# Optimization experiments

Measured on AMD Instinct MI355X. Metric: run time of the kernel, lower is better.

The kernel has to match this reference:

```python
import jax, jax.numpy as jnp
import numpy as np
import math

NUM_SYN = 1000
NUM_MEM = 100
TAU_MIN, TAU_MAX = 10.0, 1000.0
TAU_S = 5.0
DELTA_T = 1.0
LAMBDA = 3.0

def _kappas():
    kappa_s = np.float32(np.exp(-DELTA_T / TAU_S))  # scalar (tau_s uniform)
    tau_m = np.logspace(math.log10(TAU_MIN + 1e-06), math.log10(TAU_MAX - 1e-06), NUM_MEM)
    kappa_m = np.exp(-DELTA_T / np.clip(tau_m, 1e-06, None)).astype(np.float32)
    return kappa_s, jnp.asarray(kappa_m)

def custom_tanh(x):
    return jnp.tanh(x * (2.0 / 3.0)) * 1.7159

def setup_inputs() -> dict:
    key = jax.random.key(0)
    ks = jax.random.split(key, 5)
    B, T = 128, 1024
    H = 2 * NUM_MEM  # 200
    X = jax.random.normal(ks[0], (B, T, NUM_SYN), dtype=jnp.float32)
    w_s = jnp.full((NUM_SYN,), 0.5, dtype=jnp.float32)
    W1 = jax.random.normal(ks[1], (NUM_SYN + NUM_MEM, H), dtype=jnp.float32) * 0.03
    b1 = jnp.zeros((H,), dtype=jnp.float32)
    W2 = jax.random.normal(ks[2], (H, NUM_MEM), dtype=jnp.float32) * 0.07
    b2 = jnp.zeros((NUM_MEM,), dtype=jnp.float32)
    Wy = jax.random.normal(ks[3], (NUM_MEM, 10), dtype=jnp.float32) * 0.1
    by = jnp.zeros((10,), dtype=jnp.float32)
    return {"X": X, "w_s": w_s, "W1": W1, "b1": b1, "W2": W2, "b2": b2, "Wy": Wy, "by": by}

def reference(X, w_s, W1, b1, W2, b2, Wy, by):
    kappa_s, kappa_m = _kappas()
    B = X.shape[0]
    w_s_pos = jax.nn.relu(w_s)

    def step(carry, x_t):
        s, m = carry  # s: [B, S], m: [B, M]
        s = kappa_s * s + w_s_pos * x_t
        km = kappa_m * m
        inp = jnp.concatenate([s, km], axis=-1)  # [B, S+M]
        h = jax.nn.relu(inp @ W1 + b1)
        dm = custom_tanh(h @ W2 + b2)
        m = km + LAMBDA * (1.0 - kappa_m) * dm
        y = m @ Wy + by
        return (s, m), y

    s0 = jnp.zeros((B, NUM_SYN), dtype=X.dtype)
    m0 = jnp.zeros((B, NUM_MEM), dtype=X.dtype)
    Xt = jnp.swapaxes(X, 0, 1)  # [T, B, S]
    _, ys = jax.lax.scan(step, (s0, m0), Xt)
    return jnp.swapaxes(ys, 0, 1)  # [B, T, num_output]
```

## Files before the change

### kernel.cpp

```cpp
#include <hip/hip_runtime.h>
#include <math.h>

#define SDIM 1000
#define KPAD 1024
#define HDIM 200
#define MDIM 100
#define NPAD 208
#define TSTEPS 1024
#define BATCH 128
#define MT (BATCH*TSTEPS)
#define TOTX ((size_t)MT*(size_t)SDIM)

#define Z_OFF 458752

typedef _Float16 half2_t __attribute__((ext_vector_type(2)));
typedef __attribute__((ext_vector_type(8))) short short8;
typedef __attribute__((ext_vector_type(4))) float f32x4;

static __device__ __forceinline__ unsigned short f2bf(float f) {
    unsigned u = __float_as_uint(f);
    unsigned r = 0x7fffu + ((u >> 16) & 1u);
    return (unsigned short)((u + r) >> 16);
}
static __device__ __forceinline__ float bf2f(unsigned short h) {
    return __uint_as_float((unsigned)h << 16);
}
static __device__ __forceinline__ half2_t as_h2(unsigned v) {
    union { unsigned u; half2_t h; } c; c.u = v; return c.h;
}
static __device__ __forceinline__ unsigned as_u32(half2_t h) {
    union { half2_t h; unsigned u; } c; c.h = h; return c.u;
}
static __device__ __forceinline__ half2_t pk2(float a, float b) {
    half2_t r; r[0] = (_Float16)a; r[1] = (_Float16)b; return r;
}

static __device__ __forceinline__ void wg_barrier() {
    asm volatile("s_waitcnt lgkmcnt(0)" ::: "memory");
    __builtin_amdgcn_s_barrier();
    asm volatile("" ::: "memory");
}

__global__ __launch_bounds__(256) void prep_wpt(const float* __restrict__ w_s,
                                                const float* __restrict__ W1,
                                                unsigned short* __restrict__ wpt) {
    int idx = blockIdx.x * 256 + threadIdx.x;
    int n = idx >> 10, k = idx & (KPAD - 1);
    float v = 0.f;
    if (n < HDIM && k < SDIM) {
        float ws = fmaxf(w_s[k], 0.f);
        v = ws * W1[k * HDIM + n];
    }
    wpt[idx] = f2bf(v);
}

__global__ __launch_bounds__(256) void gemm_z(const float* __restrict__ X,
                                              const unsigned short* __restrict__ wpt,
                                              unsigned short* __restrict__ Z) {
    __shared__ __align__(16) unsigned short Abuf[2][128][40];
    __shared__ __align__(16) unsigned short Bbuf[2][13][16][40];
    const int t = threadIdx.x;
    const int m0 = blockIdx.x * 128;
    const int lane = t & 63, w = t >> 6;

    f32x4 acc[2][13];
#pragma unroll
    for (int mt = 0; mt < 2; ++mt)
#pragma unroll
        for (int i = 0; i < 13; ++i) acc[mt][i] = (f32x4){0.f, 0.f, 0.f, 0.f};

    auto stageA = [&](int bsel, int k0) {
        const int row = t >> 1, half = t & 1;
        size_t g = (size_t)(m0 + row) * SDIM + (size_t)(k0 + half * 16);
        float4 f0{}, f1{}, f2{}, f3{};
        if (g + 15 < TOTX) {
            f0 = *(const float4*)(X + g);      f1 = *(const float4*)(X + g + 4);
            f2 = *(const float4*)(X + g + 8);  f3 = *(const float4*)(X + g + 12);
        }
        short8 p0, p1;
        p0[0]=(short)f2bf(f0.x); p0[1]=(short)f2bf(f0.y); p0[2]=(short)f2bf(f0.z); p0[3]=(short)f2bf(f0.w);
        p0[4]=(short)f2bf(f1.x); p0[5]=(short)f2bf(f1.y); p0[6]=(short)f2bf(f1.z); p0[7]=(short)f2bf(f1.w);
        p1[0]=(short)f2bf(f2.x); p1[1]=(short)f2bf(f2.y); p1[2]=(short)f2bf(f2.z); p1[3]=(short)f2bf(f2.w);
        p1[4]=(short)f2bf(f3.x); p1[5]=(short)f2bf(f3.y); p1[6]=(short)f2bf(f3.z); p1[7]=(short)f2bf(f3.w);
        *(short8*)&Abuf[bsel][row][half * 16]     = p0;
        *(short8*)&Abuf[bsel][row][half * 16 + 8] = p1;
    };
    auto stageB = [&](int bsel, int k0) {
#pragma unroll
        for (int j = 0; j < 4; ++j) {
            int e = t + 256 * j;
            if (e < 832) {
                int n = e >> 2, q = e & 3;
                short8 v = *(const short8*)(wpt + (size_t)n * KPAD + k0 + q * 8);
                *(short8*)&Bbuf[bsel][n >> 4][n & 15][q * 8] = v;
            }
        }
    };

    stageA(0, 0);
    stageB(0, 0);
#pragma unroll 1
    for (int it = 0; it < 32; ++it) {
        __syncthreads();
        if (it + 1 < 32) { stageA((it + 1) & 1, (it + 1) * 32); stageB((it + 1) & 1, (it + 1) * 32); }
        const int bsel = it & 1;
        const short8 av0 = *(const short8*)&Abuf[bsel][w * 32 + (lane & 15)][(lane >> 4) * 8];
        const short8 av1 = *(const short8*)&Abuf[bsel][w * 32 + 16 + (lane & 15)][(lane >> 4) * 8];
#pragma unroll
        for (int nt = 0; nt < 13; ++nt) {
            const short8 bv = *(const short8*)&Bbuf[bsel][nt][lane & 15][(lane >> 4) * 8];
            acc[0][nt] = __builtin_amdgcn_mfma_f32_16x16x32_bf16(av0, bv, acc[0][nt], 0, 0, 0);
            acc[1][nt] = __builtin_amdgcn_mfma_f32_16x16x32_bf16(av1, bv, acc[1][nt], 0, 0, 0);
        }
    }

    const int colb = lane & 15;
#pragma unroll
    for (int mt = 0; mt < 2; ++mt) {
        const int rowb = m0 + w * 32 + mt * 16 + (lane >> 4) * 4;
#pragma unroll
        for (int nt = 0; nt < 13; ++nt) {
            int col = nt * 16 + colb;
            if (col < HDIM) {
#pragma unroll
                for (int r = 0; r < 4; ++r)
                    Z[(size_t)(rowb + r) * HDIM + col] = f2bf(acc[mt][nt][r]);
            }
        }
    }
}

__global__ __launch_bounds__(256, 1) void scan_seq(const unsigned short* __restrict__ Z,
        const float* __restrict__ W1, const float* __restrict__ b1,
        const float* __restrict__ W2, const float* __restrict__ b2,
        const float* __restrict__ Wy, const float* __restrict__ by,
        float* __restrict__ out) {
    __shared__ __align__(16) float part[2][4][104];
    __shared__ float kap_s[104], cm_s[104];

    const int t = threadIdx.x;
    const int b = blockIdx.x;
    const int w = t >> 6, lane = t & 63;
    const int n = 50 * w + lane;
    const bool hAct = lane < 50;
    const bool yAct = (w == 0) && (lane >= 50 && lane < 60);
    const int o = lane - 50;

    if (t < 104) {
        float kv = 0.f, cv = 0.f;
        if (t < MDIM) {
            double lg = 1.0000000434294482
                      + (double)t * ((2.9999999995657055 - 1.0000000434294482) / 99.0);
            double tau = exp(lg * 2.302585092994046);
            kv = (float)exp(-1.0 / tau);
            cv = 3.0f * (1.0f - kv);
        }
        kap_s[t] = kv; cm_s[t] = cv;
    }
    __syncthreads();

    half2_t w1r[50];
#pragma unroll
    for (int c = 0; c < 50; ++c) {
        float a0 = 0.f, a1 = 0.f;
        if (hAct) {
            a0 = kap_s[2 * c]     * W1[(SDIM + 2 * c)     * HDIM + n];
            a1 = kap_s[2 * c + 1] * W1[(SDIM + 2 * c + 1) * HDIM + n];
        } else if (yAct) {
            a0 = Wy[(2 * c) * 10 + o];
            a1 = Wy[(2 * c + 1) * 10 + o];
        }
        w1r[c] = pk2(a0, a1);
    }
    float base_b = hAct ? b1[n] : (yAct ? by[o] : 0.f);

    const int j0 = 2 * lane, j1 = 2 * lane + 1;
    half2_t w2r[50];
#pragma unroll
    for (int c = 0; c < 25; ++c) {
        float a00 = 0.f, a10 = 0.f, a01 = 0.f, a11 = 0.f;
        if (hAct) {
            int k0 = 50 * w + 2 * c, k1 = k0 + 1;
            a00 = W2[k0 * MDIM + j0]; a10 = W2[k1 * MDIM + j0];
            a01 = W2[k0 * MDIM + j1]; a11 = W2[k1 * MDIM + j1];
        }
        w2r[2 * c]     = pk2(a00, a10);
        w2r[2 * c + 1] = pk2(a01, a11);
    }

    float kap0 = 0.f, kap1 = 0.f, cm0 = 0.f, cm1 = 0.f, b20 = 0.f, b21 = 0.f;
    if (hAct) {
        kap0 = kap_s[j0]; kap1 = kap_s[j1];
        cm0 = cm_s[j0];   cm1 = cm_s[j1];
        b20 = b2[j0];     b21 = b2[j1];
    }

    const unsigned short* Zb = Z + (size_t)b * TSTEPS * HDIM;
    float* outb = out + (size_t)b * TSTEPS * 10;

    float u = 0.f, m0 = 0.f, m1 = 0.f;
    unsigned short zA = 0, zB = 0;
    if (hAct) { zA = Zb[n]; zB = Zb[HDIM + n]; }

    int sm[50];
#pragma unroll
    for (int c = 0; c < 50; ++c) sm[c] = 0;

    __syncthreads();

    auto stepf = [&](const int P, unsigned short& zreg, const int st) {
        float acc = base_b;
        if (hAct) {
            u = 0.81873075307798182f * u + bf2f(zreg);
            int stn = st + 2; stn = (stn < TSTEPS) ? stn : TSTEPS - 1;
            zreg = Zb[(size_t)stn * HDIM + n];
            acc += u;
        }
        float r = acc;
        if (hAct || yAct) {
#pragma unroll
            for (int c = 0; c < 50; ++c)
                r = __builtin_amdgcn_fdot2(w1r[c], as_h2((unsigned)sm[c]), r, false);
        }
        if (yAct && st > 0) outb[(size_t)(st - 1) * 10 + o] = r;
        float h = fmaxf(r, 0.f);

        float ho = __shfl_xor(h, 1);
        unsigned hpk = as_u32(pk2(h, ho));
        int sh[25];
#pragma unroll
        for (int c = 0; c < 25; ++c) sh[c] = __builtin_amdgcn_readlane((int)hpk, 2 * c);

        if (hAct) {
            float a0 = 0.f, a1 = 0.f;
#pragma unroll
            for (int c = 0; c < 25; ++c) {
                a0 = __builtin_amdgcn_fdot2(w2r[2 * c],     as_h2((unsigned)sh[c]), a0, false);
                a1 = __builtin_amdgcn_fdot2(w2r[2 * c + 1], as_h2((unsigned)sh[c]), a1, false);
            }
            *(float2*)&part[P][w][j0] = make_float2(a0, a1);
        }
        wg_barrier();

        if (hAct) {
            float2 q0 = *(const float2*)&part[P][0][j0];
            float2 q1 = *(const float2*)&part[P][1][j0];
            float2 q2 = *(const float2*)&part[P][2][j0];
            float2 q3 = *(const float2*)&part[P][3][j0];
            float s0 = ((q0.x + q1.x) + (q2.x + q3.x)) + b20;
            float s1 = ((q0.y + q1.y) + (q2.y + q3.y)) + b21;
            float x0 = s0 * (2.f / 3.f), x1 = s1 * (2.f / 3.f);
            float e0 = __expf(2.f * x0), e1 = __expf(2.f * x1);
            float dm0 = 1.7159f * (1.f - 2.f / (e0 + 1.f));
            float dm1 = 1.7159f * (1.f - 2.f / (e1 + 1.f));
            m0 = kap0 * m0 + cm0 * dm0;
            m1 = kap1 * m1 + cm1 * dm1;
        }
        unsigned mpk = as_u32(pk2(m0, m1));
#pragma unroll
        for (int c = 0; c < 50; ++c) sm[c] = __builtin_amdgcn_readlane((int)mpk, c);
    };

#pragma unroll 1
    for (int st = 0; st < TSTEPS; st += 2) {
        stepf(0, zA, st);
        stepf(1, zB, st + 1);
    }

    if (yAct) {
        float r = base_b;
#pragma unroll
        for (int c = 0; c < 50; ++c)
            r = __builtin_amdgcn_fdot2(w1r[c], as_h2((unsigned)sm[c]), r, false);
        outb[(size_t)(TSTEPS - 1) * 10 + o] = r;
    }
}

extern "C" void kernel_launch(void* const* d_in, const int* in_sizes, int n_in,
                              void* d_out, int out_size, void* d_ws, size_t ws_size,
                              hipStream_t stream) {
    const float* X  = (const float*)d_in[0];
    const float* ws = (const float*)d_in[1];
    const float* W1 = (const float*)d_in[2];
    const float* b1 = (const float*)d_in[3];
    const float* W2 = (const float*)d_in[4];
    const float* b2 = (const float*)d_in[5];
    const float* Wy = (const float*)d_in[6];
    const float* by = (const float*)d_in[7];
    float* out = (float*)d_out;

    unsigned short* wpt = (unsigned short*)d_ws;
    unsigned short* Z   = (unsigned short*)((char*)d_ws + Z_OFF);

    hipLaunchKernelGGL(prep_wpt, dim3((NPAD * KPAD) / 256), dim3(256), 0, stream, ws, W1, wpt);
    hipLaunchKernelGGL(gemm_z, dim3(MT / 128), dim3(256), 0, stream, X, wpt, Z);
    hipLaunchKernelGGL(scan_seq, dim3(BATCH), dim3(256), 0, stream,
                       Z, W1, b1, W2, b2, Wy, by, out);
}
```

Baseline: 1.038 ms.

## Batch 16 sequences per block in scan and use MFMA for recurrent matmuls

Replaces the per-sequence scan kernel (one block per batch element using fdot2 and readlane broadcasts) with a kernel that processes 16 batch elements per block. The recurrent W1, W2 and Wy products become 16x16x32 f16 MFMA operations, with h and m exchanged through LDS. This cuts the launch to 8 blocks, trading parallelism across CUs for much denser per-step math. The tanh is also rewritten using exp2 and rcp with a prescaled bias.

```diff
diff --git a/kernel.cpp b/kernel.cpp
--- a/kernel.cpp
+++ b/kernel.cpp
@@ -14,6 +14,7 @@
 #define Z_OFF 458752
 
 typedef _Float16 half2_t __attribute__((ext_vector_type(2)));
+typedef _Float16 f16x8 __attribute__((ext_vector_type(8)));
 typedef __attribute__((ext_vector_type(8))) short short8;
 typedef __attribute__((ext_vector_type(4))) float f32x4;
 
@@ -21,18 +22,6 @@
     unsigned u = __float_as_uint(f);
     unsigned r = 0x7fffu + ((u >> 16) & 1u);
     return (unsigned short)((u + r) >> 16);
-}
-static __device__ __forceinline__ float bf2f(unsigned short h) {
-    return __uint_as_float((unsigned)h << 16);
-}
-static __device__ __forceinline__ half2_t as_h2(unsigned v) {
-    union { unsigned u; half2_t h; } c; c.u = v; return c.h;
-}
-static __device__ __forceinline__ unsigned as_u32(half2_t h) {
-    union { half2_t h; unsigned u; } c; c.h = h; return c.u;
-}
-static __device__ __forceinline__ half2_t pk2(float a, float b) {
-    half2_t r; r[0] = (_Float16)a; r[1] = (_Float16)b; return r;
 }
 
 static __device__ __forceinline__ void wg_barrier() {
@@ -130,149 +119,236 @@
     }
 }
 
-__global__ __launch_bounds__(256, 1) void scan_seq(const unsigned short* __restrict__ Z,
+#define MSTR 136
+#define HSTR 232
+#define KEXP 1.9235933878519513f
+#define KSF  0.81873075307798182f
+
+__global__ __launch_bounds__(256, 1) void scan_mfma(
+        const unsigned short* __restrict__ Z,
         const float* __restrict__ W1, const float* __restrict__ b1,
         const float* __restrict__ W2, const float* __restrict__ b2,
         const float* __restrict__ Wy, const float* __restrict__ by,
         float* __restrict__ out) {
-    __shared__ __align__(16) float part[2][4][104];
-    __shared__ float kap_s[104], cm_s[104];
+    __shared__ __align__(16) _Float16 mbuf[16 * MSTR];
+    __shared__ __align__(16) _Float16 hbuf[16 * HSTR];
+    __shared__ float kap_s[128];
 
     const int t = threadIdx.x;
-    const int b = blockIdx.x;
+    const int bg = blockIdx.x;
     const int w = t >> 6, lane = t & 63;
-    const int n = 50 * w + lane;
-    const bool hAct = lane < 50;
-    const bool yAct = (w == 0) && (lane >= 50 && lane < 60);
-    const int o = lane - 50;
-
-    if (t < 104) {
-        float kv = 0.f, cv = 0.f;
+    const int c = lane & 15, g = lane >> 4;
+
+    if (t < 128) {
+        float kv = 0.f;
         if (t < MDIM) {
             double lg = 1.0000000434294482
                       + (double)t * ((2.9999999995657055 - 1.0000000434294482) / 99.0);
             double tau = exp(lg * 2.302585092994046);
             kv = (float)exp(-1.0 / tau);
-            cv = 3.0f * (1.0f - kv);
-        }
-        kap_s[t] = kv; cm_s[t] = cv;
-    }
+        }
+        kap_s[t] = kv;
+    }
+    for (int idx = t; idx < 16 * MSTR; idx += 256) mbuf[idx] = (_Float16)0.f;
+    for (int idx = t; idx < 16 * HSTR; idx += 256) hbuf[idx] = (_Float16)0.f;
     __syncthreads();
 
-    half2_t w1r[50];
-#pragma unroll
-    for (int c = 0; c < 50; ++c) {
-        float a0 = 0.f, a1 = 0.f;
-        if (hAct) {
-            a0 = kap_s[2 * c]     * W1[(SDIM + 2 * c)     * HDIM + n];
-            a1 = kap_s[2 * c + 1] * W1[(SDIM + 2 * c + 1) * HDIM + n];
-        } else if (yAct) {
-            a0 = Wy[(2 * c) * 10 + o];
-            a1 = Wy[(2 * c + 1) * 10 + o];
-        }
-        w1r[c] = pk2(a0, a1);
-    }
-    float base_b = hAct ? b1[n] : (yAct ? by[o] : 0.f);
-
-    const int j0 = 2 * lane, j1 = 2 * lane + 1;
-    half2_t w2r[50];
-#pragma unroll
-    for (int c = 0; c < 25; ++c) {
-        float a00 = 0.f, a10 = 0.f, a01 = 0.f, a11 = 0.f;
-        if (hAct) {
-            int k0 = 50 * w + 2 * c, k1 = k0 + 1;
-            a00 = W2[k0 * MDIM + j0]; a10 = W2[k1 * MDIM + j0];
-            a01 = W2[k0 * MDIM + j1]; a11 = W2[k1 * MDIM + j1];
-        }
-        w2r[2 * c]     = pk2(a00, a10);
-        w2r[2 * c + 1] = pk2(a01, a11);
-    }
-
-    float kap0 = 0.f, kap1 = 0.f, cm0 = 0.f, cm1 = 0.f, b20 = 0.f, b21 = 0.f;
-    if (hAct) {
-        kap0 = kap_s[j0]; kap1 = kap_s[j1];
-        cm0 = cm_s[j0];   cm1 = cm_s[j1];
-        b20 = b2[j0];     b21 = b2[j1];
-    }
-
-    const unsigned short* Zb = Z + (size_t)b * TSTEPS * HDIM;
-    float* outb = out + (size_t)b * TSTEPS * 10;
-
-    float u = 0.f, m0 = 0.f, m1 = 0.f;
-    unsigned short zA = 0, zB = 0;
-    if (hAct) { zA = Zb[n]; zB = Zb[HDIM + n]; }
-
-    int sm[50];
-#pragma unroll
-    for (int c = 0; c < 50; ++c) sm[c] = 0;
-
+    const int base1 = (w == 0) ? 0 : (1 + 3 * w);
+    const int n1 = (w == 0) ? 4 : 3;
+    const int base2 = 2 * w;
+    const int n2 = (w == 3) ? 1 : 2;
+    const bool isw3 = (w == 3);
+
+    f16x8 w1f[4][4];
+    float b1c[4][4];
+    f32x4 u[4];
+#pragma unroll
+    for (int i = 0; i < 4; ++i) {
+        const int T = base1 + i;
+        const int n = 16 * T + c;
+        const bool tv = (i < n1);
+#pragma unroll
+        for (int ks = 0; ks < 4; ++ks)
+#pragma unroll
+            for (int e = 0; e < 8; ++e) {
+                int k = 32 * ks + 8 * g + e;
+                float v = (tv && k < MDIM && n < HDIM)
+                        ? kap_s[k] * W1[(SDIM + k) * HDIM + n] : 0.f;
+                w1f[i][ks][e] = (_Float16)v;
+            }
+#pragma unroll
+        for (int r = 0; r < 4; ++r) {
+            int nr = 16 * T + 4 * g + r;
+            b1c[i][r] = (tv && nr < HDIM) ? b1[nr] : 0.f;
+        }
+        u[i] = (f32x4){0.f, 0.f, 0.f, 0.f};
+    }
+
+    f16x8 w2f[2][7];
+    float kapc[2][4], cmc[2][4], b2kc[2][4], mst[2][4];
+#pragma unroll
+    for (int j = 0; j < 2; ++j) {
+        const int Tj = base2 + j;
+        const int mj = 16 * Tj + c;
+        const bool jv = (j < n2);
+#pragma unroll
+        for (int ks = 0; ks < 7; ++ks)
+#pragma unroll
+            for (int e = 0; e < 8; ++e) {
+                int k = 32 * ks + 8 * g + e;
+                float v = (jv && k < HDIM && mj < MDIM) ? W2[k * MDIM + mj] : 0.f;
+                w2f[j][ks][e] = (_Float16)v;
+            }
+#pragma unroll
+        for (int r = 0; r < 4; ++r) {
+            int mr = 16 * Tj + 4 * g + r;
+            bool mv = jv && (mr < MDIM);
+            float kv = mv ? kap_s[mr] : 0.f;
+            kapc[j][r] = kv;
+            cmc[j][r]  = mv ? 3.f * (1.f - kv) : 0.f;
+            b2kc[j][r] = mv ? b2[mr] * KEXP : 0.f;
+            mst[j][r]  = 0.f;
+        }
+    }
+
+    f16x8 wyf[4];
+    float byc[4];
+#pragma unroll
+    for (int ks = 0; ks < 4; ++ks)
+#pragma unroll
+        for (int e = 0; e < 8; ++e) {
+            int k = 32 * ks + 8 * g + e;
+            wyf[ks][e] = (_Float16)((isw3 && c < 10 && k < MDIM) ? Wy[k * 10 + c] : 0.f);
+        }
+#pragma unroll
+    for (int r = 0; r < 4; ++r) {
+        int o = 4 * g + r;
+        byc[r] = (isw3 && o < 10) ? by[o] : 0.f;
+    }
+
+    const unsigned short* Zc = Z + (size_t)(bg * 16 + c) * (TSTEPS * HDIM);
+    float* outc = out + (size_t)(bg * 16 + c) * (TSTEPS * 10);
+
+    uint2 zA[4], zB[4];
+#pragma unroll
+    for (int i = 0; i < 4; ++i) {
+        const int n0 = 16 * (base1 + i) + 4 * g;
+        const bool zv = (i < n1) && (n0 < HDIM);
+        zA[i] = zv ? *(const uint2*)(Zc + 0 * HDIM + n0) : make_uint2(0u, 0u);
+        zB[i] = zv ? *(const uint2*)(Zc + 1 * HDIM + n0) : make_uint2(0u, 0u);
+    }
     __syncthreads();
 
-    auto stepf = [&](const int P, unsigned short& zreg, const int st) {
-        float acc = base_b;
-        if (hAct) {
-            u = 0.81873075307798182f * u + bf2f(zreg);
-            int stn = st + 2; stn = (stn < TSTEPS) ? stn : TSTEPS - 1;
-            zreg = Zb[(size_t)stn * HDIM + n];
-            acc += u;
-        }
-        float r = acc;
-        if (hAct || yAct) {
-#pragma unroll
-            for (int c = 0; c < 50; ++c)
-                r = __builtin_amdgcn_fdot2(w1r[c], as_h2((unsigned)sm[c]), r, false);
-        }
-        if (yAct && st > 0) outb[(size_t)(st - 1) * 10 + o] = r;
-        float h = fmaxf(r, 0.f);
-
-        float ho = __shfl_xor(h, 1);
-        unsigned hpk = as_u32(pk2(h, ho));
-        int sh[25];
-#pragma unroll
-        for (int c = 0; c < 25; ++c) sh[c] = __builtin_amdgcn_readlane((int)hpk, 2 * c);
-
-        if (hAct) {
-            float a0 = 0.f, a1 = 0.f;
-#pragma unroll
-            for (int c = 0; c < 25; ++c) {
-                a0 = __builtin_amdgcn_fdot2(w2r[2 * c],     as_h2((unsigned)sh[c]), a0, false);
-                a1 = __builtin_amdgcn_fdot2(w2r[2 * c + 1], as_h2((unsigned)sh[c]), a1, false);
-            }
-            *(float2*)&part[P][w][j0] = make_float2(a0, a1);
+    auto stepf = [&](uint2 (&zr)[4], const int st) {
+        f16x8 bm[4];
+#pragma unroll
+        for (int ks = 0; ks < 4; ++ks)
+            bm[ks] = *(const f16x8*)(&mbuf[c * MSTR + 8 * g + 32 * ks]);
+
+        f32x4 acc1[4];
+#pragma unroll
+        for (int i = 0; i < 4; ++i) {
+            uint2 zv = zr[i];
+            u[i][0] = fmaf(KSF, u[i][0], __uint_as_float(zv.x << 16));
+            u[i][1] = fmaf(KSF, u[i][1], __uint_as_float(zv.x & 0xffff0000u));
+            u[i][2] = fmaf(KSF, u[i][2], __uint_as_float(zv.y << 16));
+            u[i][3] = fmaf(KSF, u[i][3], __uint_as_float(zv.y & 0xffff0000u));
+            acc1[i][0] = u[i][0] + b1c[i][0];
+            acc1[i][1] = u[i][1] + b1c[i][1];
+            acc1[i][2] = u[i][2] + b1c[i][2];
+            acc1[i][3] = u[i][3] + b1c[i][3];
+            const int n0 = 16 * (base1 + i) + 4 * g;
+            if ((i < n1) && (n0 < HDIM)) {
+                int stn = st + 2; stn = (stn < TSTEPS) ? stn : TSTEPS - 1;
+                zr[i] = *(const uint2*)(Zc + (size_t)stn * HDIM + n0);
+            }
+        }
+
+#pragma unroll
+        for (int i = 0; i < 4; ++i) {
+            if (i < n1) {
+#pragma unroll
+                for (int ks = 0; ks < 4; ++ks)
+                    acc1[i] = __builtin_amdgcn_mfma_f32_16x16x32_f16(
+                                  w1f[i][ks], bm[ks], acc1[i], 0, 0, 0);
+            }
+        }
+
+        if (isw3) {
+            f32x4 ya = (f32x4){0.f, 0.f, 0.f, 0.f};
+#pragma unroll
+            for (int ks = 0; ks < 4; ++ks)
+                ya = __builtin_amdgcn_mfma_f32_16x16x32_f16(wyf[ks], bm[ks], ya, 0, 0, 0);
+            if (st > 0) {
+#pragma unroll
+                for (int r = 0; r < 4; ++r) {
+                    int o = 4 * g + r;
+                    if (o < 10)
+                        outc[(size_t)(st - 1) * 10 + o] = ya[r] + byc[r];
+                }
+            }
+        }
+
+#pragma unroll
+        for (int i = 0; i < 4; ++i) {
+            if (i < n1) {
+                unsigned p0 = __builtin_bit_cast(unsigned,
+                    __builtin_amdgcn_cvt_pkrtz(fmaxf(acc1[i][0], 0.f), fmaxf(acc1[i][1], 0.f)));
+                unsigned p1 = __builtin_bit_cast(unsigned,
+                    __builtin_amdgcn_cvt_pkrtz(fmaxf(acc1[i][2], 0.f), fmaxf(acc1[i][3], 0.f)));
+                *(uint2*)(&hbuf[c * HSTR + 16 * (base1 + i) + 4 * g]) = make_uint2(p0, p1);
+            }
         }
         wg_barrier();
 
-        if (hAct) {
-            float2 q0 = *(const float2*)&part[P][0][j0];
-            float2 q1 = *(const float2*)&part[P][1][j0];
-            float2 q2 = *(const float2*)&part[P][2][j0];
-            float2 q3 = *(const float2*)&part[P][3][j0];
-            float s0 = ((q0.x + q1.x) + (q2.x + q3.x)) + b20;
-            float s1 = ((q0.y + q1.y) + (q2.y + q3.y)) + b21;
-            float x0 = s0 * (2.f / 3.f), x1 = s1 * (2.f / 3.f);
-            float e0 = __expf(2.f * x0), e1 = __expf(2.f * x1);
-            float dm0 = 1.7159f * (1.f - 2.f / (e0 + 1.f));
-            float dm1 = 1.7159f * (1.f - 2.f / (e1 + 1.f));
-            m0 = kap0 * m0 + cm0 * dm0;
-            m1 = kap1 * m1 + cm1 * dm1;
-        }
-        unsigned mpk = as_u32(pk2(m0, m1));
-#pragma unroll
-        for (int c = 0; c < 50; ++c) sm[c] = __builtin_amdgcn_readlane((int)mpk, c);
+        f16x8 bh[7];
+#pragma unroll
+        for (int ks = 0; ks < 7; ++ks)
+            bh[ks] = *(const f16x8*)(&hbuf[c * HSTR + 8 * g + 32 * ks]);
+#pragma unroll
+        for (int j = 0; j < 2; ++j) {
+            if (j < n2) {
+                f32x4 a2 = (f32x4){0.f, 0.f, 0.f, 0.f};
+#pragma unroll
+                for (int ks = 0; ks < 7; ++ks)
+                    a2 = __builtin_amdgcn_mfma_f32_16x16x32_f16(w2f[j][ks], bh[ks], a2, 0, 0, 0);
+#pragma unroll
+                for (int r = 0; r < 4; ++r) {
+                    float E = __builtin_amdgcn_exp2f(fmaf(a2[r], KEXP, b2kc[j][r]));
+                    float dm = 1.7159f - 3.4318f * __builtin_amdgcn_rcpf(E + 1.f);
+                    mst[j][r] = fmaf(kapc[j][r], mst[j][r], cmc[j][r] * dm);
+                }
+                unsigned q0 = __builtin_bit_cast(unsigned,
+                    __builtin_amdgcn_cvt_pkrtz(mst[j][0], mst[j][1]));
+                unsigned q1 = __builtin_bit_cast(unsigned,
+                    __builtin_amdgcn_cvt_pkrtz(mst[j][2], mst[j][3]));
+                *(uint2*)(&mbuf[c * MSTR + 16 * (base2 + j) + 4 * g]) = make_uint2(q0, q1);
+            }
+        }
+        wg_barrier();
     };
 
 #pragma unroll 1
     for (int st = 0; st < TSTEPS; st += 2) {
-        stepf(0, zA, st);
-        stepf(1, zB, st + 1);
-    }
-
-    if (yAct) {
-        float r = base_b;
-#pragma unroll
-        for (int c = 0; c < 50; ++c)
-            r = __builtin_amdgcn_fdot2(w1r[c], as_h2((unsigned)sm[c]), r, false);
-        outb[(size_t)(TSTEPS - 1) * 10 + o] = r;
+        stepf(zA, st);
+        stepf(zB, st + 1);
+    }
+
+    if (isw3) {
+        f16x8 bm[4];
+#pragma unroll
+        for (int ks = 0; ks < 4; ++ks)
+            bm[ks] = *(const f16x8*)(&mbuf[c * MSTR + 8 * g + 32 * ks]);
+        f32x4 ya = (f32x4){0.f, 0.f, 0.f, 0.f};
+#pragma unroll
+        for (int ks = 0; ks < 4; ++ks)
+            ya = __builtin_amdgcn_mfma_f32_16x16x32_f16(wyf[ks], bm[ks], ya, 0, 0, 0);
+#pragma unroll
+        for (int r = 0; r < 4; ++r) {
+            int o = 4 * g + r;
+            if (o < 10)
+                outc[(size_t)(TSTEPS - 1) * 10 + o] = ya[r] + byc[r];
+        }
     }
 }
 
@@ -294,6 +370,6 @@
 
     hipLaunchKernelGGL(prep_wpt, dim3((NPAD * KPAD) / 256), dim3(256), 0, stream, ws, W1, wpt);
     hipLaunchKernelGGL(gemm_z, dim3(MT / 128), dim3(256), 0, stream, X, wpt, Z);
-    hipLaunchKernelGGL(scan_seq, dim3(BATCH), dim3(256), 0, stream,
+    hipLaunchKernelGGL(scan_mfma, dim3(BATCH / 16), dim3(256), 0, stream,
                        Z, W1, b1, W2, b2, Wy, by, out);
 }
```

After: 1.597 ms. 53.8% more time.
